# Kernel optimization log

Hardware: AMD Instinct MI355X
Metric: run time of the kernel (lower is better)

Reference implementation:

```python
import jax, jax.numpy as jnp
import numpy as np

EPS_OT = 0.05   # sinkhorn epsilon
ITERS = 3       # sinkhorn iterations
NH = 8          # attention heads


def _l2norm(x, axis):
    return x / jnp.maximum(jnp.linalg.norm(x, axis=axis, keepdims=True), 1e-12)


def _conv(x, w, pad):
    return jax.lax.conv_general_dilated(
        x, w, (1, 1), ((pad, pad), (pad, pad)),
        dimension_numbers=("NCHW", "OIHW", "NCHW"))


def _head(x, w1, b1, g, beta, w2, b2):
    # Conv3x3 -> BatchNorm (train-mode batch stats) -> ReLU -> Conv1x1
    h = _conv(x, w1, 1) + b1[None, :, None, None]
    mu = jnp.mean(h, (0, 2, 3), keepdims=True)
    var = jnp.var(h, (0, 2, 3), keepdims=True)
    h = jax.nn.relu((h - mu) / jnp.sqrt(var + 1e-5) * g[None, :, None, None]
                    + beta[None, :, None, None])
    return jnp.einsum("oc,bchw->bohw", w2, h) + b2[None, :, None, None]


def setup_inputs() -> dict:
    key = jax.random.key(0)
    ks = jax.random.split(key, 20)
    B, C, H, W, TD = 8, 256, 48, 48, 512
    s = 0.02
    f32 = jnp.float32
    d = {
        "img_feat": jax.random.normal(ks[0], (B, C, H, W), f32),
        "txt_feat": jax.random.normal(ks[1], (B, TD), f32),
        "density_map": jax.random.uniform(ks[2], (B, 1, H, W), f32),
        "tp_w": s * jax.random.normal(ks[3], (C, TD), f32), "tp_b": jnp.zeros((C,), f32),
        "wq": s * jax.random.normal(ks[4], (C, C), f32), "bq": jnp.zeros((C,), f32),
        "wk": s * jax.random.normal(ks[5], (C, C), f32), "bk": jnp.zeros((C,), f32),
        "wv": s * jax.random.normal(ks[6], (C, C), f32), "bv": jnp.zeros((C,), f32),
        "wo": s * jax.random.normal(ks[7], (C, C), f32), "bo": jnp.zeros((C,), f32),
        "ln_g": jnp.ones((C,), f32), "ln_b": jnp.zeros((C,), f32),
        "op_w": s * jax.random.normal(ks[8], (C, C), f32), "op_b": jnp.zeros((C,), f32),
        "h1_w": s * jax.random.normal(ks[9], (C // 2, C, 3, 3), f32), "h1_b": jnp.zeros((C // 2,), f32),
        "h_bn_g": jnp.ones((C // 2,), f32), "h_bn_b": jnp.zeros((C // 2,), f32),
        "h2_w": s * jax.random.normal(ks[10], (2, C // 2), f32), "h2_b": jnp.zeros((2,), f32),
        "v1_w": s * jax.random.normal(ks[11], (C // 2, C, 3, 3), f32), "v1_b": jnp.zeros((C // 2,), f32),
        "v_bn_g": jnp.ones((C // 2,), f32), "v_bn_b": jnp.zeros((C // 2,), f32),
        "v2_w": s * jax.random.normal(ks[12], (2, C // 2), f32), "v2_b": jnp.zeros((2,), f32),
        "temperature": 0.07 * jnp.ones((1,), f32),
        "spatial_weight": 0.1 * jnp.ones((1,), f32),
    }
    return d


def reference(img_feat, txt_feat, density_map, tp_w, tp_b, wq, bq, wk, bk,
              wv, bv, wo, bo, ln_g, ln_b, op_w, op_b, h1_w, h1_b, h_bn_g,
              h_bn_b, h2_w, h2_b, v1_w, v1_b, v_bn_g, v_bn_b, v2_w, v2_b,
              temperature, spatial_weight):
    B, C, H, W = img_feat.shape
    N = H * W
    hd = C // NH

    # ---- text projection (single text token) ----
    txt_emb = txt_feat @ tp_w.T + tp_b                      # [B,C]

    # ---- cross attention: query = pixels, key/value = 1 text token ----
    img_flat = img_feat.reshape(B, C, N).transpose(0, 2, 1)  # [B,N,C]
    q = (img_flat @ wq.T + bq).reshape(B, N, NH, hd)
    k = (txt_emb @ wk.T + bk).reshape(B, 1, NH, hd)
    v = (txt_emb @ wv.T + bv).reshape(B, 1, NH, hd)
    scores = jnp.einsum("bnhd,bkhd->bhnk", q, k) / jnp.sqrt(jnp.float32(hd))
    attn = jax.nn.softmax(scores, axis=-1)                  # ones (k len = 1)
    ctx = jnp.einsum("bhnk,bkhd->bnhd", attn, v).reshape(B, N, C)
    attn_out = ctx @ wo.T + bo

    # ---- residual + layernorm ----
    x = img_flat + attn_out
    mu = jnp.mean(x, -1, keepdims=True)
    var = jnp.var(x, -1, keepdims=True)
    source_feat = (x - mu) / jnp.sqrt(var + 1e-5) * ln_g + ln_b   # [B,N,C]
    mod_img_feat = source_feat.transpose(0, 2, 1).reshape(B, C, H, W)

    # ---- target distribution q from density map ----
    target = jax.nn.relu(density_map.reshape(B, N)) + 1e-6
    q_dist = target / jnp.sum(target, axis=1, keepdims=True)

    # ---- source distribution p from cosine similarity ----
    img_n = _l2norm(mod_img_feat, 1)                        # [B,C,H,W]
    txt_n = _l2norm(txt_emb, 1)                             # [B,C]
    cos = jnp.sum(img_n * txt_n[:, :, None, None], axis=1).reshape(B, N)
    temp = jnp.clip(temperature, 0.01, None)                # [1]
    logits = cos / temp
    mask = (cos > 0.0).astype(jnp.float32)
    shifted = logits - jnp.max(logits, axis=1, keepdims=True)
    p_un = jnp.exp(shifted) * mask + 1e-8
    p = p_un / jnp.sum(p_un, axis=1, keepdims=True)

    # ---- cost matrix: feature + spatial ----
    src_n = _l2norm(source_feat, 2)                         # [B,N,C]
    feature_cost = 1.0 - jnp.einsum("bnc,bmc->bnm", src_n, src_n)
    gy, gx = jnp.meshgrid(jnp.linspace(0.0, 1.0, H), jnp.linspace(0.0, 1.0, W),
                          indexing="ij")
    coords = jnp.stack([gy, gx], -1).reshape(N, 2)
    d2 = jnp.sum((coords[:, None, :] - coords[None, :, :]) ** 2, -1)
    spatial_cost = jnp.sqrt(jnp.maximum(d2, 0.0)) / 1.41421356  # [N,N]
    cost = feature_cost + spatial_weight * spatial_cost[None]   # [B,N,N]

    # ---- log-domain Sinkhorn ----
    log_p = jnp.log(p + 1e-12)
    log_q = jnp.log(q_dist + 1e-12)
    f = jnp.zeros_like(p)
    g = jnp.zeros_like(q_dist)
    for _ in range(ITERS):
        f = EPS_OT * (log_p - jax.scipy.special.logsumexp(
            (g[:, None, :] - cost) / EPS_OT, axis=2))
        g = EPS_OT * (log_q - jax.scipy.special.logsumexp(
            (f[:, :, None] - cost) / EPS_OT, axis=1))
    T = jnp.exp((f[:, :, None] + g[:, None, :] - cost) / EPS_OT)

    # ---- transport features: T^T @ source ----
    fused = jnp.einsum("bnm,bnc->bmc", T, source_feat)      # [B,N,C]
    fused_feat = fused.transpose(0, 2, 1).reshape(B, C, H, W)

    out_feat = img_feat + (jnp.einsum("oc,bchw->bohw", op_w, fused_feat)
                           + op_b[None, :, None, None])
    heatmap_logits = _head(out_feat, h1_w, h1_b, h_bn_g, h_bn_b, h2_w, h2_b)
    hv_logits = _head(out_feat, v1_w, v1_b, v_bn_g, v_bn_b, v2_w, v2_b)
    return out_feat, heatmap_logits, hv_logits
```

## Files before the change

### kernel.cpp

```cpp
#include <hip/hip_runtime.h>
#include <hip/hip_bf16.h>

#define NTOK 2304
#define CCH  256
#define BB   8
#define NSPL 2

typedef __attribute__((ext_vector_type(4))) float f32x4;
typedef __attribute__((ext_vector_type(8))) short s16x8;
typedef __attribute__((ext_vector_type(8))) _Float16 h16x8;
typedef unsigned short u16;
typedef unsigned char u8;

__device__ __forceinline__ u16 f2bf(float x){
  union{float f; unsigned u;} v; v.f = x;
  unsigned r = v.u + 0x7fffu + ((v.u>>16)&1u);
  return (u16)(r>>16);
}
__device__ __forceinline__ float bf2f(u16 h){
  union{float f; unsigned u;} v; v.u = ((unsigned)h)<<16; return v.f;
}

#if __has_builtin(__builtin_amdgcn_cvt_f32_fp8) && __has_builtin(__builtin_amdgcn_cvt_pk_fp8_f32)
#define HWFP8 1
#else
#define HWFP8 0
#endif

__device__ __forceinline__ u8 enc8(float z){
  union{float f; unsigned u;} a; a.f = fabsf(z) * 0x1p-120f;
  unsigned u = a.u + 0x7FFFFu + ((a.u>>20)&1u);
  unsigned b = (u>>20)&0x7Fu;
  if (b > 0x7Eu) b = 0x7Eu;
  return (u8)(b | (z<0.f ? 0x80u : 0u));
}
__device__ __forceinline__ float dec8(unsigned b){
  union{unsigned u; float f;} w;
  w.u = ((b&0x80u)<<24) | ((b&0x7Fu)<<20);
  return w.f * 0x1p120f;
}

#if HWFP8
__device__ __forceinline__ float DEC8(unsigned w, int e){
  switch(e & 3){
    case 0:  return __builtin_amdgcn_cvt_f32_fp8((int)w, 0);
    case 1:  return __builtin_amdgcn_cvt_f32_fp8((int)w, 1);
    case 2:  return __builtin_amdgcn_cvt_f32_fp8((int)w, 2);
    default: return __builtin_amdgcn_cvt_f32_fp8((int)w, 3);
  }
}
__device__ __forceinline__ unsigned pack4(float z0,float z1,float z2,float z3){
  int v = __builtin_amdgcn_cvt_pk_fp8_f32(z0, z1, 0, false);
  v = __builtin_amdgcn_cvt_pk_fp8_f32(z2, z3, v, true);
  return (unsigned)v;
}
#else
__device__ __forceinline__ float DEC8(unsigned w, int e){
  return dec8((w>>(8*(e&3)))&0xFFu);
}
__device__ __forceinline__ unsigned pack4(float z0,float z1,float z2,float z3){
  return (unsigned)enc8(z0) | ((unsigned)enc8(z1)<<8) |
         ((unsigned)enc8(z2)<<16) | ((unsigned)enc8(z3)<<24);
}
#endif

__device__ __forceinline__ int swz512(int row, int b){ return row*512 + (b ^ ((row&7)<<4)); }
__device__ __forceinline__ int swz128(int row, int b){ return row*128 + (b ^ ((row&7)<<4)); }
__device__ __forceinline__ int swz64 (int row, int b){ return row*64  + (b ^ ((row&3)<<4)); }

__device__ __forceinline__ void gl_lds16(const void* g, void* l){
  __builtin_amdgcn_global_load_lds(
      (const __attribute__((address_space(1))) unsigned int*)g,
      (__attribute__((address_space(3))) unsigned int*)l, 16, 0, 0);
}

struct CanonArgs {
  const void* src[31];
  int n[31];
  int off[31];
};

__global__ void k_detect(const u16* probe, int* flag){
  if (threadIdx.x==0){
    int cnt=0;
    for (int i=0;i<16;++i){
      unsigned e = (probe[2*i]>>7)&0xFFu;
      if (e>=100u && e<=140u) ++cnt;
    }
    *flag = (cnt>=14)?1:0;
  }
}

__global__ __launch_bounds__(256) void k_canon(CanonArgs a, float* dst, const int* flag, int nt){
  int t = blockIdx.y;
  if (t>=nt) return;
  int n = a.n[t];
  const void* s = a.src[t];
  float* d = dst + a.off[t];
  bool isbf = (*flag)!=0;
  int n4 = n >> 2;
  for (int i = blockIdx.x*256+threadIdx.x; i < n4; i += gridDim.x*256){
    if (isbf){
      ushort4 v = ((const ushort4*)s)[i];
      float4 o; o.x=bf2f(v.x); o.y=bf2f(v.y); o.z=bf2f(v.z); o.w=bf2f(v.w);
      ((float4*)d)[i] = o;
    } else {
      ((float4*)d)[i] = ((const float4*)s)[i];
    }
  }
  int base = n4<<2;
  int rem = n - base;
  int i = blockIdx.x*256+threadIdx.x;
  if (i < rem)
    d[base+i] = isbf ? bf2f(((const u16*)s)[base+i]) : ((const float*)s)[base+i];
}

__global__ __launch_bounds__(256) void k_zero(float* p, int n4){
  int i = blockIdx.x*256+threadIdx.x;
  if (i < n4) ((float4*)p)[i] = (float4){0.f,0.f,0.f,0.f};
}

__global__ __launch_bounds__(256) void k_txt(const float* txt, const float* tpw, const float* tpb,
    const float* wv, const float* bv, const float* wo, const float* bo, float* TXTN, float* AVEC){
  int b=blockIdx.x, t=threadIdx.x;
  __shared__ float sT[512];
  __shared__ float sE[256];
  __shared__ float sV[256];
  __shared__ float red[4];
  sT[t]      = txt[b*512+t];
  sT[t+256]  = txt[b*512+256+t];
  __syncthreads();
  float acc = tpb[t];
  const float* wr = tpw + (size_t)t*512;
  for (int k=0;k<512;++k) acc = fmaf(sT[k], wr[k], acc);
  sE[t] = acc;
  float ss = acc*acc;
  for (int d=1; d<64; d<<=1) ss += __shfl_xor(ss, d);
  if ((t&63)==0) red[t>>6] = ss;
  __syncthreads();
  float nrm = sqrtf(red[0]+red[1]+red[2]+red[3]);
  TXTN[b*256+t] = acc / fmaxf(nrm, 1e-12f);
  float av = bv[t];
  const float* wvr = wv + (size_t)t*256;
  for (int k=0;k<256;++k) av = fmaf(sE[k], wvr[k], av);
  sV[t] = av;
  __syncthreads();
  float ao = bo[t];
  const float* wor = wo + (size_t)t*256;
  for (int k=0;k<256;++k) ao = fmaf(sV[k], wor[k], ao);
  AVEC[b*256+t] = ao;
}

__global__ __launch_bounds__(256) void k_lnfuse(const float* img, const float* AVEC, const float* lng,
    const float* lnb, const float* TXTN, u16* SF, u16* SN, float* COS){
  int b=blockIdx.y, n0=blockIdx.x*32, t=threadIdx.x;
  __shared__ float xt[32][256];
  float av = AVEC[b*256+t];
  const float* ip = img + ((size_t)b*256 + t)*NTOK + n0;
  #pragma unroll
  for (int j4=0;j4<8;++j4){
    float4 v = *(const float4*)(ip + j4*4);
    xt[j4*4+0][t]=v.x+av; xt[j4*4+1][t]=v.y+av; xt[j4*4+2][t]=v.z+av; xt[j4*4+3][t]=v.w+av;
  }
  int wv_=t>>6, l=t&63;
  float lg[4], lb[4], tn[4];
  #pragma unroll
  for (int k=0;k<4;++k){ lg[k]=lng[l+64*k]; lb[k]=lnb[l+64*k]; tn[k]=TXTN[b*256+l+64*k]; }
  __syncthreads();
  for (int rr=0; rr<8; ++rr){
    int j = wv_*8+rr; int n = n0+j;
    float x[4]; float s=0.f, ss=0.f;
    #pragma unroll
    for (int k=0;k<4;++k){ float v=xt[j][l+64*k]; x[k]=v; s+=v; ss=fmaf(v,v,ss); }
    for (int d=1; d<64; d<<=1){ s += __shfl_xor(s,d); ss += __shfl_xor(ss,d); }
    float mu = s*(1.f/256.f);
    float var = ss*(1.f/256.f) - mu*mu;
    float rstd = rsqrtf(fmaxf(var,0.f)+1e-5f);
    float y[4]; float sy=0.f;
    #pragma unroll
    for (int k=0;k<4;++k){ y[k] = fmaf((x[k]-mu)*rstd, lg[k], lb[k]); sy = fmaf(y[k],y[k],sy); }
    for (int d=1; d<64; d<<=1) sy += __shfl_xor(sy,d);
    float rn = 1.f/fmaxf(sqrtf(sy),1e-12f);
    float cp = 0.f;
    size_t base = ((size_t)b*NTOK + n)*CCH;
    #pragma unroll
    for (int k=0;k<4;++k){
      float sv = y[k]*rn;
      SF[base + l+64*k] = f2bf(y[k]);
      SN[base + l+64*k] = f2bf(sv);
      cp = fmaf(sv, tn[k], cp);
    }
    for (int d=1; d<64; d<<=1) cp += __shfl_xor(cp,d);
    if (l==0) COS[b*NTOK+n] = cp;
  }
}

__global__ __launch_bounds__(256) void k_pqred(const float* COS, const float* den, const float* tmpp, float* PQS){
  int b=blockIdx.x, t=threadIdx.x;
  __shared__ float red[256];
  float temp = fmaxf(tmpp[0], 0.01f);
  float mx = -1e30f;
  for (int n=t; n<NTOK; n+=256) mx = fmaxf(mx, COS[b*NTOK+n]);
  red[t]=mx; __syncthreads();
  for (int o=128;o>0;o>>=1){ if (t<o) red[t]=fmaxf(red[t],red[t+o]); __syncthreads(); }
  float maxc = red[0]; __syncthreads();
  float sp=0.f, st=0.f;
  for (int n=t; n<NTOK; n+=256){
    float cv = COS[b*NTOK+n];
    sp += __expf((cv-maxc)/temp)*((cv>0.f)?1.f:0.f)+1e-8f;
    float dv = den[b*NTOK+n];
    st += fmaxf(dv,0.f)+1e-6f;
  }
  red[t]=sp; __syncthreads();
  for (int o=128;o>0;o>>=1){ if (t<o) red[t]+=red[t+o]; __syncthreads(); }
  sp = red[0]; __syncthreads();
  red[t]=st; __syncthreads();
  for (int o=128;o>0;o>>=1){ if (t<o) red[t]+=red[t+o]; __syncthreads(); }
  if (t==0){ PQS[b*4]=maxc; PQS[b*4+1]=sp; PQS[b*4+2]=red[0]; }
}

__global__ __launch_bounds__(256) void k_pqelem(const float* COS, const float* den, const float* tmpp,
    const float* swp, const float* PQS, float* LOGP, float* LOGQ, float* GV, u16* PJ, float* SPT){
  int idx = blockIdx.x*256+threadIdx.x;
  float temp = fmaxf(tmpp[0], 0.01f);
  if (idx < BB*NTOK){
    int b = idx / NTOK;
    float maxc = PQS[b*4], sp = PQS[b*4+1], st = PQS[b*4+2];
    float cv = COS[idx];
    float pu = __expf((cv-maxc)/temp)*((cv>0.f)?1.f:0.f)+1e-8f;
    LOGP[idx] = logf(pu/sp + 1e-12f);
    float dv = den[idx];
    LOGQ[idx] = logf((fmaxf(dv,0.f)+1e-6f)/st + 1e-12f);
    GV[idx] = 0.f;
  }
  if (idx < NTOK){
    int h = idx/48, w = idx - h*48;
    PJ[idx] = (u16)(h*95 + w);
  }
  if (idx < 9025){
    int dh = idx/95 - 47, dw = idx - (idx/95)*95 - 47;
    float spw = swp[0]*(20.0f/1.41421356f);
    float dy = (float)dh*(1.f/47.f), dx = (float)dw*(1.f/47.f);
    SPT[idx] = spw*sqrtf(fmaf(dy,dy,dx*dx));
  }
}

__global__ __launch_bounds__(256) void k_packw(const float* h1w, const float* v1w, u16* W2P){
  int idx = blockIdx.x*256+threadIdx.x;
  int kc = idx >> 14;
  int rem = idx & 16383;
  int o = rem >> 6;
  int cl = rem & 63;
  int tap = kc >> 2;
  int c = ((kc&3)<<6) + cl;
  int head = o >> 7, oc = o & 127;
  const float* src = head ? v1w : h1w;
  W2P[idx] = f2bf(src[(oc*256 + c)*9 + tap]);
}

__global__ __launch_bounds__(256) void k_trans(const u16* SF, u16* SFT){
  int n0 = blockIdx.x*64, c0 = blockIdx.y*64, b = blockIdx.z;
  __shared__ u16 tl[64][68];
  int t = threadIdx.x;
  int nl = t>>3, c8 = (t&7)*8;
  #pragma unroll
  for (int p=0;p<2;++p){
    int n = nl + p*32;
    s16x8 v = *(const s16x8*)(SF + ((size_t)(b*NTOK + n0+n)*CCH + c0 + c8));
    #pragma unroll
    for (int e=0;e<8;++e) tl[c8+e][n] = (u16)v[e];
  }
  __syncthreads();
  int cl = t>>3, n8 = (t&7)*8;
  #pragma unroll
  for (int p=0;p<2;++p){
    int c = cl + p*32;
    union{ s16x8 v; u16 us[8]; } pk;
    #pragma unroll
    for (int e=0;e<8;++e){ int s = n8+e; pk.us[e] = tl[c][((s&3)<<4) | (s>>2)]; }
    *(s16x8*)(SFT + ((size_t)(b*CCH + c0+c)*NTOK + n0 + n8)) = pk.v;
  }
}

__global__ __launch_bounds__(256, 4) void k_cost(const u16* SN, const u16* PJ, const float* SPT,
    u8* Z, float* PZ, int b_base){
  int zb = blockIdx.z, b = b_base + zb;
  int i0 = blockIdx.x*64, by = blockIdx.y, j0b = by*256;
  const u16* SNb = SN + (size_t)b*NTOK*CCH;
  u8* Zb = Z + (size_t)zb*NTOK*NTOK;
  __shared__ __align__(16) char Bs[64*512];
  int tid=threadIdx.x, w=tid>>6, l=tid&63, g4=l>>4, lc=l&15;
  const u16* Arow = SNb + (size_t)(i0 + w*16 + lc)*CCH + g4*8;
  s16x8 af[8];
  #pragma unroll
  for (int ks=0; ks<8; ++ks) af[ks] = *(const s16x8*)(Arow + ks*32);
  int mrow = w*16 + g4*4;
  int ipi[4];
  #pragma unroll
  for (int r=0;r<4;++r) ipi[r] = (int)PJ[i0+mrow+r] + 4512;
  float Srow[4] = {0.f,0.f,0.f,0.f};
  for (int js=0; js<4; ++js){
    int j0 = j0b + js*64;
    __syncthreads();
    #pragma unroll
    for (int u=0; u<8; ++u){
      int row = u*8 + w*2 + (l>>5);
      int src = ((l&31)*16) ^ ((row&7)<<4);
      gl_lds16((const char*)(SNb + (size_t)(j0+row)*CCH) + src, Bs + u*4096 + w*1024);
    }
    __syncthreads();
    f32x4 acc[4];
    #pragma unroll
    for (int cf=0;cf<4;++cf) acc[cf] = (f32x4){0.f,0.f,0.f,0.f};
    #pragma unroll
    for (int ks=0; ks<8; ++ks){
      int kb = ks*64 + g4*16;
      #pragma unroll
      for (int cf=0; cf<4; ++cf){
        s16x8 bb = *(const s16x8*)(Bs + swz512(cf*16+lc, kb));
        acc[cf] = __builtin_amdgcn_mfma_f32_16x16x32_bf16(af[ks], bb, acc[cf], 0,0,0);
      }
    }
    float zf[4][4];
    #pragma unroll
    for (int cf=0; cf<4; ++cf){
      int j = j0 + cf*16 + lc;
      int pjj = (int)PJ[j];
      #pragma unroll
      for (int r=0;r<4;++r){
        float sp = SPT[ipi[r] - pjj];
        zf[cf][r] = (acc[cf][r]-1.0f)*20.0f - sp;
      }
    }
    size_t zrow = (size_t)(i0+mrow)*NTOK + j0 + lc*4;
    #pragma unroll
    for (int r=0;r<4;++r){
      unsigned pw = pack4(zf[0][r], zf[1][r], zf[2][r], zf[3][r]);
      Srow[r] += __expf(DEC8(pw,0)) + __expf(DEC8(pw,1))
               + __expf(DEC8(pw,2)) + __expf(DEC8(pw,3));
      *(unsigned*)(Zb + zrow + (size_t)r*NTOK) = pw;
    }
  }
  #pragma unroll
  for (int r=0;r<4;++r){
    float s = Srow[r];
    s += __shfl_xor(s,1); s += __shfl_xor(s,2); s += __shfl_xor(s,4); s += __shfl_xor(s,8);
    if (lc==0) PZ[(size_t)(zb*NTOK + i0 + mrow + r)*9 + by] = s;
  }
}

__global__ __launch_bounds__(256) void k_sinkred(const float* PZ, const float* LOGP, float* FV,
    int b_base, int zcnt){
  int idx = blockIdx.x*256 + threadIdx.x;
  if (idx >= zcnt*NTOK) return;
  int zb = idx / NTOK, row = idx - zb*NTOK, b = b_base + zb;
  const float* p = PZ + (size_t)idx*9;
  float s = 0.f;
  #pragma unroll
  for (int k=0;k<9;++k) s += p[k];
  FV[b*NTOK+row] = 0.05f*(LOGP[b*NTOK+row] - logf(s));
}

__global__ __launch_bounds__(256) void k_sinkZ(const u8* Z, const float* addv,
    const float* basev, float* outv, int b_base){
  int zb = blockIdx.y, b = b_base + zb, i0 = blockIdx.x*32;
  __shared__ float fs[NTOK];
  __shared__ float wm[4];
  int t = threadIdx.x;
  for (int j=t; j<NTOK; j+=256){
    int p = j & 63, tt = ((p&3)<<4) | (p>>2);
    fs[j] = addv[b*NTOK + (j & ~63) + tt]*20.f;
  }
  __syncthreads();
  float m = -1e30f;
  for (int j=t; j<NTOK; j+=256) m = fmaxf(m, fs[j]);
  #pragma unroll
  for (int d=1; d<64; d<<=1) m = fmaxf(m, __shfl_xor(m, d));
  if ((t&63)==0) wm[t>>6] = m;
  __syncthreads();
  float C = fmaxf(fmaxf(wm[0],wm[1]), fmaxf(wm[2],wm[3]));
  __syncthreads();
  for (int j=t; j<NTOK; j+=256) fs[j] -= C;
  __syncthreads();
  int rl = t>>3, q = t&7;
  int row = i0 + rl;
  const u8* zr = Z + ((size_t)zb*NTOK + row)*NTOK;
  float S = 0.f;
  for (int c0 = q*32; c0 < NTOK; c0 += 256){
    uint4 zA = *(const uint4*)(zr + c0);
    uint4 zB = *(const uint4*)(zr + c0 + 16);
    unsigned wd[8] = {zA.x,zA.y,zA.z,zA.w, zB.x,zB.y,zB.z,zB.w};
    float s32 = 0.f;
    #pragma unroll
    for (int k=0;k<8;++k)
      #pragma unroll
      for (int e=0;e<4;++e)
        s32 += __expf(fs[c0 + k*4 + e] + DEC8(wd[k], e));
    S += s32;
  }
  #pragma unroll
  for (int d=1; d<8; d<<=1) S += __shfl_xor(S, d);
  if (q==0)
    outv[b*NTOK+row] = 0.05f*(basev[b*NTOK+row] - (C + logf(S)));
}

__global__ __launch_bounds__(256, 3) void k_applyT(const u8* Z, const u16* SFT, const float* FVv,
    const float* GVv, float* FUF, int b_base){
  int zb = blockIdx.z, b = b_base + zb, m0 = blockIdx.x*64;
  int sp = blockIdx.y;
  int nbeg = sp*(NTOK/NSPL), nend = nbeg + (NTOK/NSPL);
  __shared__ __align__(16) char WtL[64*128];
  __shared__ __align__(16) char BL[256*128];
  __shared__ float gs[64];
  __shared__ float sfv[NTOK/NSPL];
  int tid=threadIdx.x, w=tid>>6, l=tid&63, g4=l>>4, lc=l&15;
  if (tid<64) gs[tid] = GVv[b*NTOK+m0+tid]*20.f;
  const float* Fv = FVv + b*NTOK;
  for (int j=tid; j<NTOK/NSPL; j+=256){
    int jj = nbeg + j;
    int p = jj & 63, tt = ((p&3)<<4) | (p>>2);
    sfv[j] = Fv[(jj & ~63) + tt]*20.f;
  }
  const u8* Zb = Z + ((size_t)zb*NTOK + m0)*NTOK;
  const u16* SFTb = SFT + (size_t)b*CCH*NTOK;
  f32x4 acc[4][4];
  #pragma unroll
  for (int mf=0;mf<4;++mf)
    #pragma unroll
    for (int cf=0;cf<4;++cf) acc[mf][cf] = (f32x4){0.f,0.f,0.f,0.f};
  int zm = tid>>2, zq = (tid&3)*16;
  int lrow = l>>3;
  int lsrc = ((l&7)*16) ^ (lrow<<4);
  uint4 zwc = *(const uint4*)(Zb + (size_t)zm*NTOK + nbeg + zq);
  for (int n0=nbeg; n0<nend; n0+=64){
    __syncthreads();
    int nn = (n0+64 < nend) ? n0+64 : nbeg;
    uint4 zwn = *(const uint4*)(Zb + (size_t)zm*NTOK + nn + zq);
    #pragma unroll
    for (int u=0; u<8; ++u){
      int row = w*64 + u*8 + lrow;
      gl_lds16((const char*)(SFTb + (size_t)row*NTOK) + n0*2 + lsrc,
               BL + (w*64 + u*8)*128);
    }
    {
      float g20 = gs[zm];
      unsigned wd[4] = {zwc.x, zwc.y, zwc.z, zwc.w};
      union{ s16x8 v; u16 us[8]; } w0, w1;
      int sbase = n0 - nbeg + zq;
      #pragma unroll
      for (int col=0; col<16; ++col){
        float val = __expf(sfv[sbase+col] + g20 + DEC8(wd[col>>2], col&3));
        if (col < 8) w0.us[col] = f2bf(val); else w1.us[col-8] = f2bf(val);
      }
      *(s16x8*)(WtL + swz128(zm, zq*2)) = w0.v;
      *(s16x8*)(WtL + swz128(zm, zq*2+16)) = w1.v;
    }
    __syncthreads();
    #pragma unroll
    for (int kk=0; kk<2; ++kk){
      s16x8 a[4];
      #pragma unroll
      for (int mf=0;mf<4;++mf) a[mf] = *(const s16x8*)(WtL + swz128(mf*16+lc, kk*64 + g4*16));
      #pragma unroll
      for (int cf=0; cf<4; ++cf){
        s16x8 bb = *(const s16x8*)(BL + swz128(w*64+cf*16+lc, kk*64 + g4*16));
        #pragma unroll
        for (int mf=0; mf<4; ++mf)
          acc[mf][cf] = __builtin_amdgcn_mfma_f32_16x16x32_bf16(a[mf], bb, acc[mf][cf], 0,0,0);
      }
    }
    zwc = zwn;
  }
  float* FUb = FUF + (size_t)b*NTOK*CCH;
  #pragma unroll
  for (int mf=0; mf<4; ++mf)
    #pragma unroll
    for (int cf=0; cf<4; ++cf)
      #pragma unroll
      for (int r=0;r<4;++r){
        int m = m0 + mf*16 + g4*4 + r;
        int c = w*64 + cf*16 + lc;
        atomicAdd(&FUb[(size_t)m*CCH + c], acc[mf][cf][r]);
      }
}

__global__ __launch_bounds__(256) void k_opgemm(const float* FUF, const float* opw, const float* opb,
    const float* img, float* dout, u16* OFN){
  int b=blockIdx.y, n0=blockIdx.x*64;
  __shared__ __align__(16) char Am[64*512];
  __shared__ __align__(16) char Bw[256*64];
  int tid=threadIdx.x, w=tid>>6, l=tid&63, g4=l>>4, lc=l&15;
  const float* FUb = FUF + (size_t)b*NTOK*CCH;
  for (int ch=tid; ch<64*32; ch+=256){
    int r=ch>>5, c8=(ch&31)*8;
    const float* fp = FUb + (size_t)(n0+r)*CCH + c8;
    float4 v0 = *(const float4*)fp;
    float4 v1 = *(const float4*)(fp+4);
    union { s16x8 v; u16 us[8]; } pk;
    pk.us[0]=f2bf(v0.x); pk.us[1]=f2bf(v0.y); pk.us[2]=f2bf(v0.z); pk.us[3]=f2bf(v0.w);
    pk.us[4]=f2bf(v1.x); pk.us[5]=f2bf(v1.y); pk.us[6]=f2bf(v1.z); pk.us[7]=f2bf(v1.w);
    *(s16x8*)(Am + swz512(r, c8*2)) = pk.v;
  }
  f32x4 acc[4][4];
  #pragma unroll
  for (int mf=0;mf<4;++mf)
    #pragma unroll
    for (int cf=0;cf<4;++cf) acc[mf][cf] = (f32x4){0.f,0.f,0.f,0.f};
  for (int ks=0; ks<8; ++ks){
    __syncthreads();
    {
      int o = tid;
      const float* wr = opw + (size_t)o*CCH + ks*32;
      #pragma unroll
      for (int u=0; u<4; ++u){
        float4 v0 = *(const float4*)(wr + u*8);
        float4 v1 = *(const float4*)(wr + u*8 + 4);
        union { s16x8 v; u16 us[8]; } pk;
        pk.us[0]=f2bf(v0.x); pk.us[1]=f2bf(v0.y); pk.us[2]=f2bf(v0.z); pk.us[3]=f2bf(v0.w);
        pk.us[4]=f2bf(v1.x); pk.us[5]=f2bf(v1.y); pk.us[6]=f2bf(v1.z); pk.us[7]=f2bf(v1.w);
        *(s16x8*)(Bw + swz64(o, u*16)) = pk.v;
      }
    }
    __syncthreads();
    #pragma unroll
    for (int mf=0; mf<4; ++mf){
      s16x8 a = *(const s16x8*)(Am + swz512(mf*16+lc, (ks*32+g4*8)*2));
      #pragma unroll
      for (int cf=0; cf<4; ++cf){
        int o = w*64+cf*16+lc;
        s16x8 bb = *(const s16x8*)(Bw + swz64(o, g4*16));
        acc[mf][cf] = __builtin_amdgcn_mfma_f32_16x16x32_bf16(a, bb, acc[mf][cf], 0,0,0);
      }
    }
  }
  #pragma unroll
  for (int mf=0; mf<4; ++mf){
    int nl = mf*16 + g4*4; int n = n0+nl;
    #pragma unroll
    for (int cf=0; cf<4; ++cf){
      int o = w*64+cf*16+lc;
      float ob = opb[o];
      const float* ip = img + ((size_t)b*CCH + o)*NTOK + n;
      float4 im = *(const float4*)ip;
      float o0 = acc[mf][cf][0]+ob+im.x;
      float o1 = acc[mf][cf][1]+ob+im.y;
      float o2 = acc[mf][cf][2]+ob+im.z;
      float o3 = acc[mf][cf][3]+ob+im.w;
      float4 st; st.x=o0; st.y=o1; st.z=o2; st.w=o3;
      *(float4*)(dout + ((size_t)b*CCH+o)*NTOK + n) = st;
      u16* ofp = OFN + ((size_t)b*NTOK + n)*CCH + o;
      ofp[0]=f2bf(o0); ofp[CCH]=f2bf(o1); ofp[2*CCH]=f2bf(o2); ofp[3*CCH]=f2bf(o3);
    }
  }
}

__global__ __launch_bounds__(256, 2) void k_conv2(const u16* OFN, const u16* W2P,
    const float* h1b, const float* v1b, u16* H1, u16* H2){
  int b = blockIdx.y, n0 = blockIdx.x*64;
  __shared__ __align__(16) char As[64*128];
  __shared__ __align__(16) char Ws[2][256*128];
  int tid=threadIdx.x, w=tid>>6, l=tid&63, g4=l>>4, lc=l&15;
  int ar = tid>>2, aseg = (tid&3)*16;
  int arow = n0 + ar;
  int hr = arow/48, wc = arow - hr*48;
  const u16* Ob = OFN + (size_t)b*NTOK*CCH;
  int wrow = tid>>3;
  int wsrc = ((tid&7)*16) ^ ((wrow&7)<<4);
  const char* Wbase = (const char*)W2P;
  f32x4 acc[4][4];
  #pragma unroll
  for (int mf=0;mf<4;++mf)
    #pragma unroll
    for (int of=0;of<4;++of) acc[mf][of] = (f32x4){0.f,0.f,0.f,0.f};
  auto STAGEW = [&](int kc, int buf){
    const char* src = Wbase + (size_t)kc*32768;
    #pragma unroll
    for (int u=0; u<8; ++u)
      gl_lds16(src + (size_t)(u*32 + wrow)*128 + wsrc, Ws[buf] + u*4096 + w*1024);
  };
  auto LOADA = [&](int kc, s16x8& ra0, s16x8& ra1){
    int tap = kc>>2, cq = (kc&3)*64;
    int kh = tap/3;
    int dh = kh-1, dw = (tap-kh*3)-1;
    bool val = ((unsigned)(hr+dh) < 48u) && ((unsigned)(wc+dw) < 48u);
    ra0 = (s16x8){0,0,0,0,0,0,0,0}; ra1 = ra0;
    if (val){
      const u16* ap = Ob + (size_t)(arow + dh*48 + dw)*CCH + cq + aseg;
      ra0 = *(const s16x8*)ap;
      ra1 = *(const s16x8*)(ap+8);
    }
  };
  s16x8 a0, a1, na0, na1;
  STAGEW(0, 0);
  LOADA(0, a0, a1);
  for (int kc=0; kc<36; ++kc){
    int cur = kc & 1;
    __builtin_amdgcn_s_barrier();
    __builtin_amdgcn_sched_barrier(0);
    if (kc+1 < 36){
      STAGEW(kc+1, cur^1);
      LOADA(kc+1, na0, na1);
    }
    *(s16x8*)(As + swz128(ar, aseg*2))    = a0;
    *(s16x8*)(As + swz128(ar, aseg*2+16)) = a1;
    asm volatile("s_waitcnt lgkmcnt(0)" ::: "memory");
    __builtin_amdgcn_s_barrier();
    __builtin_amdgcn_sched_barrier(0);
    #pragma unroll
    for (int ks=0; ks<2; ++ks){
      s16x8 af[4];
      #pragma unroll
      for (int mf=0;mf<4;++mf) af[mf] = *(const s16x8*)(As + swz128(mf*16+lc, ks*64 + g4*16));
      #pragma unroll
      for (int of=0; of<4; ++of){
        s16x8 bf = *(const s16x8*)(Ws[cur] + swz128(w*64+of*16+lc, ks*64 + g4*16));
        #pragma unroll
        for (int mf=0; mf<4; ++mf)
          acc[mf][of] = __builtin_amdgcn_mfma_f32_16x16x32_bf16(af[mf], bf, acc[mf][of], 0,0,0);
      }
    }
    a0 = na0; a1 = na1;
  }
  #pragma unroll
  for (int of=0; of<4; ++of){
    int o = w*64 + of*16 + lc;
    int head = o>>7, oc = o&127;
    float bias = (head? v1b : h1b)[oc];
    u16* Hh = head? H2 : H1;
    #pragma unroll
    for (int mf=0; mf<4; ++mf){
      #pragma unroll
      for (int r=0;r<4;++r){
        int n = n0 + mf*16 + g4*4 + r;
        Hh[((size_t)b*NTOK+n)*128 + oc] = f2bf(acc[mf][of][r] + bias);
      }
    }
  }
}

__global__ __launch_bounds__(128) void k_stats(const u16* H1, const u16* H2, float* PART){
  int head=blockIdx.y, blk=blockIdx.x, t=threadIdx.x;
  const u16* Hh = head? H2:H1;
  float s=0.f, ss=0.f;
  size_t r0 = (size_t)blk*288;
  for (int r=0;r<288;++r){
    float v = bf2f(Hh[(r0+r)*128 + t]);
    s += v; ss = fmaf(v,v,ss);
  }
  PART[((head*64+blk)*128+t)*2]   = s;
  PART[((head*64+blk)*128+t)*2+1] = ss;
}

__global__ __launch_bounds__(128) void k_statr(const float* PART, const float* hbg, const float* hbb,
    const float* vbg, const float* vbb, float* BNS){
  int head=blockIdx.x, t=threadIdx.x;
  float s=0.f, ss=0.f;
  for (int blk=0;blk<64;++blk){
    s  += PART[((head*64+blk)*128+t)*2];
    ss += PART[((head*64+blk)*128+t)*2+1];
  }
  float mean = s*(1.f/18432.f);
  float var = ss*(1.f/18432.f) - mean*mean;
  var = fmaxf(var, 0.f);
  const float* g  = head? vbg:hbg;
  const float* be = head? vbb:hbb;
  float sc = g[t]/sqrtf(var+1e-5f);
  BNS[(head*128+t)*2]   = sc;
  BNS[(head*128+t)*2+1] = be[t] - mean*sc;
}

__global__ __launch_bounds__(128) void k_fin(const u16* H1, const u16* H2, const float* BNS,
    const float* h2w, const float* h2b, const float* v2w, const float* v2b, float* dout){
  int head = blockIdx.z, b = blockIdx.y, n0 = blockIdx.x*128, t=threadIdx.x;
  const u16* Hh = head? H2:H1;
  const float* w2 = head? v2w:h2w;
  const float* b2 = head? v2b:h2b;
  __shared__ u16 tile[128][130];
  __shared__ float sc[128], bi[128], wa[128], wb[128];
  sc[t]=BNS[(head*128+t)*2]; bi[t]=BNS[(head*128+t)*2+1];
  wa[t]=w2[t]; wb[t]=w2[128+t];
  for (int r=0;r<128;++r) tile[r][t] = Hh[((size_t)b*NTOK+n0+r)*128 + t];
  __syncthreads();
  float a0=b2[0], a1=b2[1];
  for (int ch=0; ch<128; ++ch){
    float v = fmaf(bf2f(tile[t][ch]), sc[ch], bi[ch]);
    v = fmaxf(v, 0.f);
    a0 = fmaf(wa[ch], v, a0);
    a1 = fmaf(wb[ch], v, a1);
  }
  size_t base = (size_t)8*256*2304 + (size_t)head*36864 + (size_t)b*2*2304 + n0 + t;
  dout[base]        = a0;
  dout[base+2304]   = a1;
}

extern "C" void kernel_launch(void* const* d_in, const int* in_sizes, int n_in,
                              void* d_out, int out_size, void* d_ws, size_t ws_size,
                              hipStream_t stream){
  (void)out_size;
  long off[31]; long tot=0;
  int ni = n_in < 31 ? n_in : 31;
  for (int i=0;i<ni;++i){ off[i]=tot; tot += ((long)in_sizes[i]+63)&~63L; }
  char* ws = (char*)d_ws;
  size_t pos = 0;
  auto alloc = [&](size_t bytes)->char*{
    char* p = ws+pos; pos = (pos + bytes + 255) & ~(size_t)255; return p; };
  int*   FLAG = (int*)alloc(256);
  float* TXTN = (float*)alloc(8*256*4);
  float* AVEC = (float*)alloc(8*256*4);
  float* COS  = (float*)alloc(8*2304*4);
  float* LOGP = (float*)alloc(8*2304*4);
  float* LOGQ = (float*)alloc(8*2304*4);
  float* FV   = (float*)alloc(8*2304*4);
  float* GV   = (float*)alloc(8*2304*4);
  u16*   PJ   = (u16*)alloc(2304*2);
  float* SPT  = (float*)alloc(9025*4);
  float* PQS  = (float*)alloc(8*4*4);
  float* PART = (float*)alloc(2*64*128*2*4);
  float* BNS  = (float*)alloc(2*128*2*4);
  float* PZ   = (float*)alloc((size_t)8*2304*9*4);
  u16* W2P = (u16*)alloc((size_t)36*256*64*2);
  u16* SF  = (u16*)alloc((size_t)8*2304*256*2);
  u16* SN  = (u16*)alloc((size_t)8*2304*256*2);
  u16* SFT = (u16*)alloc((size_t)8*2304*256*2);
  float* FUF = (float*)alloc((size_t)8*2304*256*4);
  u16* OFN = (u16*)alloc((size_t)8*2304*256*2);
  u16* H1  = (u16*)alloc((size_t)8*2304*128*2);
  u16* H2  = (u16*)alloc((size_t)8*2304*128*2);
  float* canon = (float*)alloc((size_t)tot*4);
  size_t zslice = (size_t)NTOK*NTOK;
  int zsl = (pos + 8*zslice + 256 <= ws_size) ? 8 : 1;
  u8* Z = (u8*)alloc((size_t)zsl*zslice);

  k_detect<<<1,64,0,stream>>>((const u16*)d_in[1], FLAG);
  CanonArgs ca;
  for (int i=0;i<ni;++i){ ca.src[i]=d_in[i]; ca.n[i]=in_sizes[i]; ca.off[i]=(int)off[i]; }
  k_canon<<<dim3(512,(unsigned)ni),256,0,stream>>>(ca, canon, FLAG, ni);
  k_zero<<<4608,256,0,stream>>>(FUF, 8*2304*256/4);

  const float* c_img = canon+off[0];
  const float* c_txt = canon+off[1];
  const float* c_den = canon+off[2];
  const float* c_tpw = canon+off[3];
  const float* c_tpb = canon+off[4];
  const float* c_wv  = canon+off[9];
  const float* c_bv  = canon+off[10];
  const float* c_wo  = canon+off[11];
  const float* c_bo  = canon+off[12];
  const float* c_lng = canon+off[13];
  const float* c_lnb = canon+off[14];
  const float* c_opw = canon+off[15];
  const float* c_opb = canon+off[16];
  const float* c_h1w = canon+off[17];
  const float* c_h1b = canon+off[18];
  const float* c_hbg = canon+off[19];
  const float* c_hbb = canon+off[20];
  const float* c_h2w = canon+off[21];
  const float* c_h2b = canon+off[22];
  const float* c_v1w = canon+off[23];
  const float* c_v1b = canon+off[24];
  const float* c_vbg = canon+off[25];
  const float* c_vbb = canon+off[26];
  const float* c_v2w = canon+off[27];
  const float* c_v2b = canon+off[28];
  const float* c_tmp = canon+off[29];
  const float* c_sw  = canon+off[30];

  k_txt<<<8,256,0,stream>>>(c_txt, c_tpw, c_tpb, c_wv, c_bv, c_wo, c_bo, TXTN, AVEC);
  k_lnfuse<<<dim3(72,8),256,0,stream>>>(c_img, AVEC, c_lng, c_lnb, TXTN, SF, SN, COS);
  k_pqred<<<8,256,0,stream>>>(COS, c_den, c_tmp, PQS);
  k_pqelem<<<80,256,0,stream>>>(COS, c_den, c_tmp, c_sw, PQS, LOGP, LOGQ, GV, PJ, SPT);
  k_packw<<<2304,256,0,stream>>>(c_h1w, c_v1w, W2P);
  k_trans<<<dim3(36,4,8),256,0,stream>>>(SF, SFT);

  if (zsl == 8){
    k_cost<<<dim3(36,9,8),256,0,stream>>>(SN, PJ, SPT, Z, PZ, 0);
    k_sinkred<<<72,256,0,stream>>>(PZ, LOGP, FV, 0, 8);
    for (int it=0; it<3; ++it){
      if (it>0) k_sinkZ<<<dim3(72,8),256,0,stream>>>(Z, GV, LOGP, FV, 0);
      k_sinkZ<<<dim3(72,8),256,0,stream>>>(Z, FV, LOGQ, GV, 0);
    }
    k_applyT<<<dim3(36,NSPL,8),256,0,stream>>>(Z, SFT, FV, GV, FUF, 0);
  } else {
    for (int bi=0; bi<8; ++bi){
      k_cost<<<dim3(36,9,1),256,0,stream>>>(SN, PJ, SPT, Z, PZ, bi);
      k_sinkred<<<9,256,0,stream>>>(PZ, LOGP, FV, bi, 1);
      for (int it=0; it<3; ++it){
        if (it>0) k_sinkZ<<<dim3(72,1),256,0,stream>>>(Z, GV, LOGP, FV, bi);
        k_sinkZ<<<dim3(72,1),256,0,stream>>>(Z, FV, LOGQ, GV, bi);
      }
      k_applyT<<<dim3(36,NSPL,1),256,0,stream>>>(Z, SFT, FV, GV, FUF, bi);
    }
  }

  k_opgemm<<<dim3(36,8),256,0,stream>>>(FUF, c_opw, c_opb, c_img, (float*)d_out, OFN);
  k_conv2<<<dim3(36,8),256,0,stream>>>(OFN, W2P, c_h1b, c_v1b, H1, H2);
  k_stats<<<dim3(64,2),128,0,stream>>>(H1, H2, PART);
  k_statr<<<2,128,0,stream>>>(PART, c_hbg, c_hbb, c_vbg, c_vbb, BNS);
  k_fin<<<dim3(18,8,2),128,0,stream>>>(H1, H2, BNS, c_h2w, c_h2b, c_v2w, c_v2b, (float*)d_out);
}
```

Before: 371.9 us.

## Build transport-weight MFMA operands in registers and split N four ways

In k_applyT each wave now loads its own Z bytes and computes the exp'd bf16 A fragments straight into registers. This removes the WtL shared tile, the gs array and one block barrier per iteration, replacing the barriers with explicit waitcnt and sched_barrier ordering. The cost is that every wave recomputes the same 64x64 exps, four times the exp work per block, and the Z prefetch across iterations is gone. NSPL goes from 2 to 4, which adds blocks for occupancy but doubles the atomicAdd traffic into FUF.

```diff
diff --git a/kernel.cpp b/kernel.cpp
--- a/kernel.cpp
+++ b/kernel.cpp
@@ -4,7 +4,7 @@
 #define NTOK 2304
 #define CCH  256
 #define BB   8
-#define NSPL 2
+#define NSPL 4
 
 typedef __attribute__((ext_vector_type(4))) float f32x4;
 typedef __attribute__((ext_vector_type(8))) short s16x8;
@@ -409,67 +409,74 @@
   int zb = blockIdx.z, b = b_base + zb, m0 = blockIdx.x*64;
   int sp = blockIdx.y;
   int nbeg = sp*(NTOK/NSPL), nend = nbeg + (NTOK/NSPL);
-  __shared__ __align__(16) char WtL[64*128];
   __shared__ __align__(16) char BL[256*128];
-  __shared__ float gs[64];
   __shared__ float sfv[NTOK/NSPL];
   int tid=threadIdx.x, w=tid>>6, l=tid&63, g4=l>>4, lc=l&15;
-  if (tid<64) gs[tid] = GVv[b*NTOK+m0+tid]*20.f;
   const float* Fv = FVv + b*NTOK;
   for (int j=tid; j<NTOK/NSPL; j+=256){
     int jj = nbeg + j;
     int p = jj & 63, tt = ((p&3)<<4) | (p>>2);
     sfv[j] = Fv[(jj & ~63) + tt]*20.f;
   }
-  const u8* Zb = Z + ((size_t)zb*NTOK + m0)*NTOK;
+  float g20r[4];
+  #pragma unroll
+  for (int mf=0;mf<4;++mf) g20r[mf] = GVv[b*NTOK + m0 + mf*16 + lc]*20.f;
+  const u8* Zb = Z + (size_t)zb*NTOK*NTOK;
+  const u8* zr[4];
+  #pragma unroll
+  for (int mf=0;mf<4;++mf) zr[mf] = Zb + (size_t)(m0 + mf*16 + lc)*NTOK;
   const u16* SFTb = SFT + (size_t)b*CCH*NTOK;
-  f32x4 acc[4][4];
-  #pragma unroll
-  for (int mf=0;mf<4;++mf)
-    #pragma unroll
-    for (int cf=0;cf<4;++cf) acc[mf][cf] = (f32x4){0.f,0.f,0.f,0.f};
-  int zm = tid>>2, zq = (tid&3)*16;
   int lrow = l>>3;
   int lsrc = ((l&7)*16) ^ (lrow<<4);
-  uint4 zwc = *(const uint4*)(Zb + (size_t)zm*NTOK + nbeg + zq);
+  f32x4 acc[4][4];
+  #pragma unroll
+  for (int mf=0;mf<4;++mf)
+    #pragma unroll
+    for (int cf=0;cf<4;++cf) acc[mf][cf] = (f32x4){0.f,0.f,0.f,0.f};
+  __syncthreads();
   for (int n0=nbeg; n0<nend; n0+=64){
-    __syncthreads();
-    int nn = (n0+64 < nend) ? n0+64 : nbeg;
-    uint4 zwn = *(const uint4*)(Zb + (size_t)zm*NTOK + nn + zq);
+    __builtin_amdgcn_sched_barrier(0);
+    asm volatile("s_waitcnt lgkmcnt(0)" ::: "memory");
+    __builtin_amdgcn_sched_barrier(0);
     #pragma unroll
     for (int u=0; u<8; ++u){
       int row = w*64 + u*8 + lrow;
       gl_lds16((const char*)(SFTb + (size_t)row*NTOK) + n0*2 + lsrc,
                BL + (w*64 + u*8)*128);
     }
-    {
-      float g20 = gs[zm];
-      unsigned wd[4] = {zwc.x, zwc.y, zwc.z, zwc.w};
-      union{ s16x8 v; u16 us[8]; } w0, w1;
-      int sbase = n0 - nbeg + zq;
-      #pragma unroll
-      for (int col=0; col<16; ++col){
-        float val = __expf(sfv[sbase+col] + g20 + DEC8(wd[col>>2], col&3));
-        if (col < 8) w0.us[col] = f2bf(val); else w1.us[col-8] = f2bf(val);
-      }
-      *(s16x8*)(WtL + swz128(zm, zq*2)) = w0.v;
-      *(s16x8*)(WtL + swz128(zm, zq*2+16)) = w1.v;
-    }
-    __syncthreads();
-    #pragma unroll
-    for (int kk=0; kk<2; ++kk){
-      s16x8 a[4];
-      #pragma unroll
-      for (int mf=0;mf<4;++mf) a[mf] = *(const s16x8*)(WtL + swz128(mf*16+lc, kk*64 + g4*16));
+    uint2 zw[4][2];
+    #pragma unroll
+    for (int mf=0;mf<4;++mf)
+      #pragma unroll
+      for (int kk=0;kk<2;++kk)
+        zw[mf][kk] = *(const uint2*)(zr[mf] + n0 + kk*32 + g4*8);
+    int sb = n0 - nbeg;
+    s16x8 a[4][2];
+    #pragma unroll
+    for (int mf=0;mf<4;++mf)
+      #pragma unroll
+      for (int kk=0;kk<2;++kk){
+        union{ s16x8 v; u16 us[8]; } aa;
+        #pragma unroll
+        for (int e=0;e<8;++e){
+          unsigned wword = (e<4) ? zw[mf][kk].x : zw[mf][kk].y;
+          float val = __expf(sfv[sb + kk*32 + g4*8 + e] + g20r[mf] + DEC8(wword, e));
+          aa.us[e] = f2bf(val);
+        }
+        a[mf][kk] = aa.v;
+      }
+    asm volatile("s_waitcnt vmcnt(0)" ::: "memory");
+    __builtin_amdgcn_sched_barrier(0);
+    #pragma unroll
+    for (int kk=0; kk<2; ++kk)
       #pragma unroll
       for (int cf=0; cf<4; ++cf){
         s16x8 bb = *(const s16x8*)(BL + swz128(w*64+cf*16+lc, kk*64 + g4*16));
         #pragma unroll
         for (int mf=0; mf<4; ++mf)
-          acc[mf][cf] = __builtin_amdgcn_mfma_f32_16x16x32_bf16(a[mf], bb, acc[mf][cf], 0,0,0);
-      }
-    }
-    zwc = zwn;
+          acc[mf][cf] = __builtin_amdgcn_mfma_f32_16x16x32_bf16(a[mf][kk], bb, acc[mf][cf], 0,0,0);
+      }
+    __builtin_amdgcn_sched_barrier(0);
   }
   float* FUb = FUF + (size_t)b*NTOK*CCH;
   #pragma unroll
```

After: 458.8 us. 1.23x slower.
